# Kernel optimization log

Hardware: AMD Instinct MI355X
Metric: run time of the kernel (lower is better)

## Reference

```python
import jax, jax.numpy as jnp
import numpy as np

B, N, M, C, H, W = 8, 16, 4, 2, 256, 256
GAMMA = 0.5   # gamma0
BETA = 1.0    # beta
EPS = 1e-8


def setup_inputs() -> dict:
    key = jax.random.key(0)
    k1, k2, k3, k4 = jax.random.split(key, 4)
    gt_arr = jax.random.randint(k1, (B, M, H, W), 0, C)
    sample_arr = jax.random.uniform(k2, (B, N, C, H, W), dtype=jnp.float32)
    prob = jax.random.uniform(k3, (B, N), dtype=jnp.float32)
    prob_gt = jax.random.uniform(k4, (B, M), dtype=jnp.float32)
    prob_gt = prob_gt / prob_gt.sum(-1, keepdims=True)  # gt mixture weights sum to 1
    sample_shape = jnp.array([4, 4], dtype=jnp.int64 if jax.config.read('jax_enable_x64') else jnp.int32)  # (K,S); unused since G0=1
    return {"gt_arr": gt_arr, "sample_arr": sample_arr, "prob": prob,
            "prob_gt": prob_gt, "sample_shape": sample_shape}


def _cost_iou(sample, gt_oh):
    # sample: (B,N,C,HW), gt_oh: (B,M,C,HW) -> cost (B,N,M)
    inter = jnp.einsum('bnch,bmch->bnmc', sample, gt_oh)
    union = sample.sum(-1)[:, :, None, :] + gt_oh.sum(-1)[:, None, :, :] - inter
    # drop background channel 0, mean over remaining channels
    return 1.0 - ((inter + 1.0) / (union + 1.0))[..., 1:].mean(-1)


def _coupling(cost, prob_gt):
    # Greedy sequential OT coupling (gamma != 1 branch), vectorized per gt column
    # via water-filling over cost-sorted samples; sequential over gt columns.
    Bn, Nn, Mn = cost.shape
    mass = 1.0 / Mn

    def per_batch(cb):  # cb: (N,M)
        order_gt = jnp.argsort(cb.min(axis=0))  # gts by their min cost

        def step(carry, i):
            rowsums, P = carry
            col = cb[:, i]                      # (N,)
            ordj = jnp.argsort(col)             # samples by cost for this gt
            caps = GAMMA - rowsums[ordj]        # remaining capacity, >= 0
            excl = jnp.cumsum(caps) - caps      # exclusive prefix of capacities
            a_sorted = jnp.clip(mass - excl, 0.0, caps)
            assign = jnp.zeros((Nn,), cb.dtype).at[ordj].set(a_sorted)
            P = P.at[:, i].set(assign)
            return (rowsums + assign, P), None

        init = (jnp.zeros((Nn,), cb.dtype), jnp.zeros((Nn, Mn), cb.dtype))
        (_, P), _ = jax.lax.scan(step, init, order_gt)
        return P

    P = jax.vmap(per_batch)(cost)
    return P * (prob_gt * Mn)[:, None, :]


def _forward(gt_arr, sample_arr, prob, prob_gt):
    Bn, Nn, Cn, Hn, Wn = sample_arr.shape
    Mn = gt_arr.shape[1]
    sample = sample_arr.reshape(Bn, Nn, Cn, Hn * Wn)
    gt_oh = jnp.transpose(
        jax.nn.one_hot(gt_arr.reshape(Bn, Mn, Hn * Wn), Cn, dtype=sample.dtype),
        (0, 1, 3, 2))                            # (B,M,C,HW)
    cost = _cost_iou(sample, gt_oh)              # (B,N,M)
    P = jax.lax.stop_gradient(_coupling(jax.lax.stop_gradient(cost), prob_gt))
    seg_loss = (P * cost).sum((1, 2)).mean()
    # KL: F.kl_div(log(prob+eps), target_prob) with 'mean' reduction (xlogy at 0)
    target = P.sum(-1)                           # (B,N)
    logp = jnp.log(prob + EPS)
    safe_t = jnp.where(target > 0, target, 1.0)
    kl = jnp.where(target > 0, target * (jnp.log(safe_t) - logp), 0.0).mean()
    loss = seg_loss + BETA * kl
    return loss, seg_loss, kl


def reference(gt_arr, sample_arr, prob, prob_gt, sample_shape):
    return _forward(gt_arr, sample_arr, prob, prob_gt)
```

## Files before the change

kernel.cpp:

```cpp
#include <hip/hip_runtime.h>
#include <math.h>

static constexpr int Bn = 8;
static constexpr int Nn = 16;
static constexpr int Mn = 4;
static constexpr int Cn = 2;
static constexpr int HWn = 256 * 256;
static constexpr int Sn = 8;
static constexpr int SEG = HWn / Sn;
#define GAMMA_F 0.5f
#define MASS_F 0.25f
#define EPS_F 1e-8f


__global__ __launch_bounds__(256) void inter_kernel(
    const float* __restrict__ sample, const int* __restrict__ gt,
    float* __restrict__ inter_part, float* __restrict__ ssum_part,
    unsigned int* __restrict__ gsum_part) {
  int blk = blockIdx.x;
  int s = blk % Sn;
  int bn = blk / Sn;
  int n = bn % Nn;
  int b = bn / Nn;

  const float* sp = sample + ((((size_t)b * Nn + n) * Cn + 1) * HWn) + (size_t)s * SEG;
  const int* gtb = gt + (size_t)b * Mn * HWn + (size_t)s * SEG;

  float ss = 0.f, im0 = 0.f, im1 = 0.f, im2 = 0.f, im3 = 0.f;
  unsigned int c0 = 0, c1 = 0, c2 = 0, c3 = 0;

  for (int i = threadIdx.x; i < SEG / 4; i += 256) {
    float4 x = reinterpret_cast<const float4*>(sp)[i];
    int4 g0 = reinterpret_cast<const int4*>(gtb + 0 * HWn)[i];
    int4 g1 = reinterpret_cast<const int4*>(gtb + 1 * HWn)[i];
    int4 g2 = reinterpret_cast<const int4*>(gtb + 2 * HWn)[i];
    int4 g3 = reinterpret_cast<const int4*>(gtb + 3 * HWn)[i];
    float xs[4] = {x.x, x.y, x.z, x.w};
    int m0[4] = {g0.x, g0.y, g0.z, g0.w};
    int m1[4] = {g1.x, g1.y, g1.z, g1.w};
    int m2[4] = {g2.x, g2.y, g2.z, g2.w};
    int m3[4] = {g3.x, g3.y, g3.z, g3.w};
#pragma unroll
    for (int e = 0; e < 4; ++e) {
      float v = xs[e];
      ss += v;
      bool b0 = (m0[e] == 1), b1 = (m1[e] == 1), b2 = (m2[e] == 1), b3 = (m3[e] == 1);
      im0 += b0 ? v : 0.0f;
      im1 += b1 ? v : 0.0f;
      im2 += b2 ? v : 0.0f;
      im3 += b3 ? v : 0.0f;
      c0 += b0; c1 += b1; c2 += b2; c3 += b3;
    }
  }

#pragma unroll
  for (int off = 32; off > 0; off >>= 1) {
    ss  += __shfl_down(ss, off);
    im0 += __shfl_down(im0, off);
    im1 += __shfl_down(im1, off);
    im2 += __shfl_down(im2, off);
    im3 += __shfl_down(im3, off);
    c0  += __shfl_down(c0, off);
    c1  += __shfl_down(c1, off);
    c2  += __shfl_down(c2, off);
    c3  += __shfl_down(c3, off);
  }

  __shared__ float sred[4][5];
  __shared__ unsigned int scnt[4][4];
  int lane = threadIdx.x & 63;
  int wv = threadIdx.x >> 6;
  if (lane == 0) {
    sred[wv][0] = ss; sred[wv][1] = im0; sred[wv][2] = im1;
    sred[wv][3] = im2; sred[wv][4] = im3;
    scnt[wv][0] = c0; scnt[wv][1] = c1; scnt[wv][2] = c2; scnt[wv][3] = c3;
  }
  __syncthreads();
  if (threadIdx.x == 0) {
    float t[5] = {0, 0, 0, 0, 0};
    for (int w = 0; w < 4; ++w)
      for (int v = 0; v < 5; ++v) t[v] += sred[w][v];
    ssum_part[(size_t)bn * Sn + s] = t[0];
    float* ip = inter_part + ((size_t)bn * Sn + s) * Mn;
    ip[0] = t[1]; ip[1] = t[2]; ip[2] = t[3]; ip[3] = t[4];
    if (n == 0) {
      unsigned int cc[4] = {0, 0, 0, 0};
      for (int w = 0; w < 4; ++w)
        for (int m = 0; m < 4; ++m) cc[m] += scnt[w][m];
      unsigned int* gp = gsum_part + ((size_t)b * Sn + s) * Mn;
      gp[0] = cc[0]; gp[1] = cc[1]; gp[2] = cc[2]; gp[3] = cc[3];
    }
  }
}

__global__ __launch_bounds__(256) void finish_kernel(
    const float* __restrict__ inter_part, const float* __restrict__ ssum_part,
    const unsigned int* __restrict__ gsum_part,
    const float* __restrict__ prob, const float* __restrict__ prob_gt,
    float* __restrict__ out) {
  __shared__ float s_cost[Bn * Nn * Mn];
  __shared__ float s_ssum[Bn * Nn];
  __shared__ float s_gsum[Bn * Mn];
  __shared__ float s_red[8];
  int tid = threadIdx.x;

  if (tid < Bn * Nn) {
    float acc = 0.f;
    for (int s = 0; s < Sn; ++s) acc += ssum_part[(size_t)tid * Sn + s];
    s_ssum[tid] = acc;
  }
  if (tid >= 128 && tid < 128 + Bn * Mn) {
    int idx = tid - 128;
    int b = idx / Mn, m = idx % Mn;
    unsigned int acc = 0;
    for (int s = 0; s < Sn; ++s) acc += gsum_part[((size_t)b * Sn + s) * Mn + m];
    s_gsum[idx] = (float)acc;
  }
  __syncthreads();

  for (int idx = tid; idx < Bn * Nn * Mn; idx += 256) {
    int m = idx % Mn;
    int bn = idx / Mn;
    int b = bn / Nn;
    float acc = 0.f;
    for (int s = 0; s < Sn; ++s) acc += inter_part[((size_t)bn * Sn + s) * Mn + m];
    float uni = s_ssum[bn] + s_gsum[b * Mn + m] - acc;
    s_cost[idx] = 1.0f - (acc + 1.0f) / (uni + 1.0f);
  }
  __syncthreads();

  float seg_part = 0.f, kl_part = 0.f;
  if (tid < Bn * Nn) {
    int b = tid >> 4;
    int n = tid & 15;
    int base = (tid & 63) & ~15;

    float4 cv = *reinterpret_cast<const float4*>(&s_cost[tid * Mn]);
    float cc0 = cv.x, cc1 = cv.y, cc2 = cv.z, cc3 = cv.w;
    float pg0 = prob_gt[b * Mn + 0], pg1 = prob_gt[b * Mn + 1];
    float pg2 = prob_gt[b * Mn + 2], pg3 = prob_gt[b * Mn + 3];

    float m0 = cc0, m1 = cc1, m2 = cc2, m3 = cc3;
#pragma unroll
    for (int off = 1; off < 16; off <<= 1) {
      m0 = fminf(m0, __shfl_xor(m0, off));
      m1 = fminf(m1, __shfl_xor(m1, off));
      m2 = fminf(m2, __shfl_xor(m2, off));
      m3 = fminf(m3, __shfl_xor(m3, off));
    }
    int r0 = (m1 < m0) + (m2 < m0) + (m3 < m0);
    int r1 = (m0 <= m1) + (m2 < m1) + (m3 < m1);
    int r2 = (m0 <= m2) + (m1 <= m2) + (m3 < m2);
    int r3 = (m0 <= m3) + (m1 <= m3) + (m2 <= m3);

    float rowsum = 0.f;
    float target = 0.f;
#pragma unroll
    for (int k = 0; k < Mn; ++k) {
      int i = (r0 == k) ? 0 : (r1 == k) ? 1 : (r2 == k) ? 2 : 3;
      float v = (i == 0) ? cc0 : (i == 1) ? cc1 : (i == 2) ? cc2 : cc3;
      float pg = (i == 0) ? pg0 : (i == 1) ? pg1 : (i == 2) ? pg2 : pg3;
      float cap = GAMMA_F - rowsum;
      float excl = 0.f;
#pragma unroll 4
      for (int j = 0; j < Nn; ++j) {
        float vj = __shfl(v, base + j);
        float capj = __shfl(cap, base + j);
        bool pred = (vj < v) || (vj == v && j < n);
        excl += pred ? capj : 0.f;
      }
      float a = fminf(fmaxf(MASS_F - excl, 0.f), cap);
      rowsum += a;
      float p = a * pg * (float)Mn;
      seg_part += p * v;
      target += p;
    }
    kl_part = (target > 0.f)
                  ? target * (logf(target) - logf(prob[tid] + EPS_F))
                  : 0.f;
  }

#pragma unroll
  for (int off = 32; off > 0; off >>= 1) {
    seg_part += __shfl_down(seg_part, off);
    kl_part += __shfl_down(kl_part, off);
  }
  int lane = tid & 63, wv = tid >> 6;
  if (lane == 0) { s_red[wv * 2] = seg_part; s_red[wv * 2 + 1] = kl_part; }
  __syncthreads();
  if (tid == 0) {
    float seg = 0.f, kl = 0.f;
    for (int w = 0; w < 4; ++w) { seg += s_red[w * 2]; kl += s_red[w * 2 + 1]; }
    seg /= (float)Bn;
    kl /= (float)(Bn * Nn);
    out[0] = seg + 1.0f * kl;
    out[1] = seg;
    out[2] = kl;
  }
}

extern "C" void kernel_launch(void* const* d_in, const int* in_sizes, int n_in,
                              void* d_out, int out_size, void* d_ws, size_t ws_size,
                              hipStream_t stream) {
  const int* gt = (const int*)d_in[0];
  const float* sample = (const float*)d_in[1];
  const float* prob = (const float*)d_in[2];
  const float* prob_gt = (const float*)d_in[3];
  float* out = (float*)d_out;

  char* ws = (char*)d_ws;
  float* inter_part = (float*)(ws + 0);
  float* ssum_part = (float*)(ws + 16384);
  unsigned int* gsum_part = (unsigned int*)(ws + 20480);

  inter_kernel<<<Bn * Nn * Sn, 256, 0, stream>>>(sample, gt, inter_part, ssum_part, gsum_part);
  finish_kernel<<<1, 256, 0, stream>>>(inter_part, ssum_part, gsum_part, prob, prob_gt, out);
}
```

Baseline: 20.68 us.

## Process all samples per block to reuse ground-truth masks across samples

Restructures the reduction kernel so each block covers one batch and pixel segment for all 16 samples, with each wave handling 4 samples. Ground-truth masks are loaded once per wave and converted to float masks used via FMA, instead of being re-read for every sample. Partial sums switch to a layout with 64 segments and are reduced in shared memory, and the finish kernel sums the longer segment rows with float4 loads. The cost is more per-thread registers and a larger partial buffer, and gt is still read four times per block.

```diff
diff --git a/kernel.cpp b/kernel.cpp
--- a/kernel.cpp
+++ b/kernel.cpp
@@ -6,96 +6,118 @@
 static constexpr int Mn = 4;
 static constexpr int Cn = 2;
 static constexpr int HWn = 256 * 256;
-static constexpr int Sn = 8;
-static constexpr int SEG = HWn / Sn;
+static constexpr int SEGS = 64;
+static constexpr int SEGLEN = HWn / SEGS;
 #define GAMMA_F 0.5f
 #define MASS_F 0.25f
 #define EPS_F 1e-8f
 
 
-__global__ __launch_bounds__(256) void inter_kernel(
+__global__ __launch_bounds__(256) void inter2_kernel(
     const float* __restrict__ sample, const int* __restrict__ gt,
     float* __restrict__ inter_part, float* __restrict__ ssum_part,
-    unsigned int* __restrict__ gsum_part) {
-  int blk = blockIdx.x;
-  int s = blk % Sn;
-  int bn = blk / Sn;
-  int n = bn % Nn;
-  int b = bn / Nn;
-
-  const float* sp = sample + ((((size_t)b * Nn + n) * Cn + 1) * HWn) + (size_t)s * SEG;
-  const int* gtb = gt + (size_t)b * Mn * HWn + (size_t)s * SEG;
-
-  float ss = 0.f, im0 = 0.f, im1 = 0.f, im2 = 0.f, im3 = 0.f;
-  unsigned int c0 = 0, c1 = 0, c2 = 0, c3 = 0;
-
-  for (int i = threadIdx.x; i < SEG / 4; i += 256) {
-    float4 x = reinterpret_cast<const float4*>(sp)[i];
-    int4 g0 = reinterpret_cast<const int4*>(gtb + 0 * HWn)[i];
-    int4 g1 = reinterpret_cast<const int4*>(gtb + 1 * HWn)[i];
-    int4 g2 = reinterpret_cast<const int4*>(gtb + 2 * HWn)[i];
-    int4 g3 = reinterpret_cast<const int4*>(gtb + 3 * HWn)[i];
-    float xs[4] = {x.x, x.y, x.z, x.w};
-    int m0[4] = {g0.x, g0.y, g0.z, g0.w};
-    int m1[4] = {g1.x, g1.y, g1.z, g1.w};
-    int m2[4] = {g2.x, g2.y, g2.z, g2.w};
-    int m3[4] = {g3.x, g3.y, g3.z, g3.w};
-#pragma unroll
-    for (int e = 0; e < 4; ++e) {
-      float v = xs[e];
-      ss += v;
-      bool b0 = (m0[e] == 1), b1 = (m1[e] == 1), b2 = (m2[e] == 1), b3 = (m3[e] == 1);
-      im0 += b0 ? v : 0.0f;
-      im1 += b1 ? v : 0.0f;
-      im2 += b2 ? v : 0.0f;
-      im3 += b3 ? v : 0.0f;
-      c0 += b0; c1 += b1; c2 += b2; c3 += b3;
-    }
-  }
-
-#pragma unroll
-  for (int off = 32; off > 0; off >>= 1) {
-    ss  += __shfl_down(ss, off);
-    im0 += __shfl_down(im0, off);
-    im1 += __shfl_down(im1, off);
-    im2 += __shfl_down(im2, off);
-    im3 += __shfl_down(im3, off);
-    c0  += __shfl_down(c0, off);
-    c1  += __shfl_down(c1, off);
-    c2  += __shfl_down(c2, off);
-    c3  += __shfl_down(c3, off);
-  }
-
-  __shared__ float sred[4][5];
-  __shared__ unsigned int scnt[4][4];
-  int lane = threadIdx.x & 63;
-  int wv = threadIdx.x >> 6;
-  if (lane == 0) {
-    sred[wv][0] = ss; sred[wv][1] = im0; sred[wv][2] = im1;
-    sred[wv][3] = im2; sred[wv][4] = im3;
-    scnt[wv][0] = c0; scnt[wv][1] = c1; scnt[wv][2] = c2; scnt[wv][3] = c3;
-  }
-  __syncthreads();
-  if (threadIdx.x == 0) {
-    float t[5] = {0, 0, 0, 0, 0};
-    for (int w = 0; w < 4; ++w)
-      for (int v = 0; v < 5; ++v) t[v] += sred[w][v];
-    ssum_part[(size_t)bn * Sn + s] = t[0];
-    float* ip = inter_part + ((size_t)bn * Sn + s) * Mn;
-    ip[0] = t[1]; ip[1] = t[2]; ip[2] = t[3]; ip[3] = t[4];
-    if (n == 0) {
-      unsigned int cc[4] = {0, 0, 0, 0};
-      for (int w = 0; w < 4; ++w)
-        for (int m = 0; m < 4; ++m) cc[m] += scnt[w][m];
-      unsigned int* gp = gsum_part + ((size_t)b * Sn + s) * Mn;
-      gp[0] = cc[0]; gp[1] = cc[1]; gp[2] = cc[2]; gp[3] = cc[3];
-    }
+    float* __restrict__ gsum_part) {
+  int seg = blockIdx.x & (SEGS - 1);
+  int b = blockIdx.x >> 6;
+  int tid = threadIdx.x;
+  int w = tid >> 6;
+  int lane = tid & 63;
+  size_t segoff = (size_t)seg * SEGLEN;
+
+  const int* gtb = gt + ((size_t)b * Mn) * HWn + segoff;
+  const float* sb = sample + (size_t)b * Nn * Cn * HWn + HWn + segoff;
+
+  float ss[4] = {0.f, 0.f, 0.f, 0.f};
+  float im[4][4] = {};
+  float cnt[4] = {0.f, 0.f, 0.f, 0.f};
+
+#pragma unroll
+  for (int q = 0; q < 4; ++q) {
+    int idx = q * 64 + lane;
+    int4 g0 = reinterpret_cast<const int4*>(gtb + 0 * HWn)[idx];
+    int4 g1 = reinterpret_cast<const int4*>(gtb + 1 * HWn)[idx];
+    int4 g2 = reinterpret_cast<const int4*>(gtb + 2 * HWn)[idx];
+    int4 g3 = reinterpret_cast<const int4*>(gtb + 3 * HWn)[idx];
+    float mf[4][4];
+    {
+      int a0[4] = {g0.x, g0.y, g0.z, g0.w};
+      int a1[4] = {g1.x, g1.y, g1.z, g1.w};
+      int a2[4] = {g2.x, g2.y, g2.z, g2.w};
+      int a3[4] = {g3.x, g3.y, g3.z, g3.w};
+#pragma unroll
+      for (int e = 0; e < 4; ++e) {
+        mf[e][0] = (a0[e] == 1) ? 1.f : 0.f;
+        mf[e][1] = (a1[e] == 1) ? 1.f : 0.f;
+        mf[e][2] = (a2[e] == 1) ? 1.f : 0.f;
+        mf[e][3] = (a3[e] == 1) ? 1.f : 0.f;
+      }
+    }
+#pragma unroll
+    for (int m = 0; m < 4; ++m)
+      cnt[m] += (mf[0][m] + mf[1][m]) + (mf[2][m] + mf[3][m]);
+#pragma unroll
+    for (int nn = 0; nn < 4; ++nn) {
+      const float* spn = sb + (size_t)(w * 4 + nn) * (Cn * HWn);
+      float4 x = reinterpret_cast<const float4*>(spn)[idx];
+      float xs[4] = {x.x, x.y, x.z, x.w};
+#pragma unroll
+      for (int e = 0; e < 4; ++e) {
+        float v = xs[e];
+        ss[nn] += v;
+#pragma unroll
+        for (int m = 0; m < 4; ++m) im[nn][m] = fmaf(v, mf[e][m], im[nn][m]);
+      }
+    }
+  }
+
+  __shared__ __align__(16) float red[4][20][68];
+  __shared__ __align__(16) float redc[4][68];
+#pragma unroll
+  for (int nn = 0; nn < 4; ++nn) {
+    red[w][nn * 5 + 0][lane] = ss[nn];
+#pragma unroll
+    for (int m = 0; m < 4; ++m) red[w][nn * 5 + 1 + m][lane] = im[nn][m];
+  }
+  if (w == 0) {
+#pragma unroll
+    for (int m = 0; m < 4; ++m) redc[m][lane] = cnt[m];
+  }
+  __syncthreads();
+
+  if (tid < 80) {
+    int rw = tid / 20, v = tid % 20;
+    const float4* row = reinterpret_cast<const float4*>(&red[rw][v][0]);
+    float4 a4 = row[0];
+#pragma unroll
+    for (int j = 1; j < 16; ++j) {
+      float4 t = row[j];
+      a4.x += t.x; a4.y += t.y; a4.z += t.z; a4.w += t.w;
+    }
+    float s = (a4.x + a4.y) + (a4.z + a4.w);
+    int n = rw * 4 + v / 5;
+    int k = v % 5;
+    int bn = b * Nn + n;
+    if (k == 0)
+      ssum_part[(size_t)bn * SEGS + seg] = s;
+    else
+      inter_part[((size_t)bn * Mn + (k - 1)) * SEGS + seg] = s;
+  } else if (tid < 84) {
+    int m = tid - 80;
+    const float4* row = reinterpret_cast<const float4*>(&redc[m][0]);
+    float4 a4 = row[0];
+#pragma unroll
+    for (int j = 1; j < 16; ++j) {
+      float4 t = row[j];
+      a4.x += t.x; a4.y += t.y; a4.z += t.z; a4.w += t.w;
+    }
+    float s = (a4.x + a4.y) + (a4.z + a4.w);
+    gsum_part[((size_t)b * Mn + m) * SEGS + seg] = s;
   }
 }
 
 __global__ __launch_bounds__(256) void finish_kernel(
     const float* __restrict__ inter_part, const float* __restrict__ ssum_part,
-    const unsigned int* __restrict__ gsum_part,
+    const float* __restrict__ gsum_part,
     const float* __restrict__ prob, const float* __restrict__ prob_gt,
     float* __restrict__ out) {
   __shared__ float s_cost[Bn * Nn * Mn];
@@ -105,27 +127,41 @@
   int tid = threadIdx.x;
 
   if (tid < Bn * Nn) {
-    float acc = 0.f;
-    for (int s = 0; s < Sn; ++s) acc += ssum_part[(size_t)tid * Sn + s];
-    s_ssum[tid] = acc;
-  }
-  if (tid >= 128 && tid < 128 + Bn * Mn) {
+    const float4* row = reinterpret_cast<const float4*>(&ssum_part[(size_t)tid * SEGS]);
+    float4 a4 = row[0];
+#pragma unroll
+    for (int j = 1; j < 16; ++j) {
+      float4 t = row[j];
+      a4.x += t.x; a4.y += t.y; a4.z += t.z; a4.w += t.w;
+    }
+    s_ssum[tid] = (a4.x + a4.y) + (a4.z + a4.w);
+  } else if (tid < 128 + Bn * Mn) {
     int idx = tid - 128;
-    int b = idx / Mn, m = idx % Mn;
-    unsigned int acc = 0;
-    for (int s = 0; s < Sn; ++s) acc += gsum_part[((size_t)b * Sn + s) * Mn + m];
-    s_gsum[idx] = (float)acc;
+    const float4* row = reinterpret_cast<const float4*>(&gsum_part[(size_t)idx * SEGS]);
+    float4 a4 = row[0];
+#pragma unroll
+    for (int j = 1; j < 16; ++j) {
+      float4 t = row[j];
+      a4.x += t.x; a4.y += t.y; a4.z += t.z; a4.w += t.w;
+    }
+    s_gsum[idx] = (a4.x + a4.y) + (a4.z + a4.w);
   }
   __syncthreads();
 
   for (int idx = tid; idx < Bn * Nn * Mn; idx += 256) {
-    int m = idx % Mn;
-    int bn = idx / Mn;
-    int b = bn / Nn;
-    float acc = 0.f;
-    for (int s = 0; s < Sn; ++s) acc += inter_part[((size_t)bn * Sn + s) * Mn + m];
-    float uni = s_ssum[bn] + s_gsum[b * Mn + m] - acc;
-    s_cost[idx] = 1.0f - (acc + 1.0f) / (uni + 1.0f);
+    int m = idx & 3;
+    int bn = idx >> 2;
+    int b = bn >> 4;
+    const float4* row = reinterpret_cast<const float4*>(&inter_part[(size_t)idx * SEGS]);
+    float4 a4 = row[0];
+#pragma unroll
+    for (int j = 1; j < 16; ++j) {
+      float4 t = row[j];
+      a4.x += t.x; a4.y += t.y; a4.z += t.z; a4.w += t.w;
+    }
+    float inter = (a4.x + a4.y) + (a4.z + a4.w);
+    float uni = s_ssum[bn] + s_gsum[(b << 2) + m] - inter;
+    s_cost[idx] = 1.0f - (inter + 1.0f) / (uni + 1.0f);
   }
   __syncthreads();
 
@@ -210,9 +246,9 @@
 
   char* ws = (char*)d_ws;
   float* inter_part = (float*)(ws + 0);
-  float* ssum_part = (float*)(ws + 16384);
-  unsigned int* gsum_part = (unsigned int*)(ws + 20480);
-
-  inter_kernel<<<Bn * Nn * Sn, 256, 0, stream>>>(sample, gt, inter_part, ssum_part, gsum_part);
+  float* ssum_part = (float*)(ws + 131072);
+  float* gsum_part = (float*)(ws + 163840);
+
+  inter2_kernel<<<Bn * SEGS, 256, 0, stream>>>(sample, gt, inter_part, ssum_part, gsum_part);
   finish_kernel<<<1, 256, 0, stream>>>(inter_part, ssum_part, gsum_part, prob, prob_gt, out);
 }
```

Measured after the change: 23.29 us. +12.6%, slower.
